# Kernel tuning notes

Measured on AMD Instinct MI355X. Metric: run time of the kernel, lower is better.

Reference implementation:

```python
import jax, jax.numpy as jnp
import numpy as np

B, N, T, S, H = 8, 10000, 2000, 12, 128
BIN_SIGMA = 0.1
GAUSS_NORM = 0.3989422804  # 1/sqrt(2*pi), as hard-coded in the source


def setup_inputs() -> dict:
    key = jax.random.key(0)
    ks = jax.random.split(key, 8)
    # (x, y, z): x,y in detector mm, z already expressed in waveform-tick units
    scale = jnp.array([400.0, 400.0, float(T - 1)], dtype=jnp.float32)
    diffused_electrons = jax.random.uniform(ks[0], (B, N, 3), dtype=jnp.float32) * scale
    mask = jax.random.uniform(ks[1], (B, N), dtype=jnp.float32)  # per-electron weights
    W1 = jax.random.normal(ks[2], (3, H), dtype=jnp.float32) * (1.0 / np.sqrt(3.0))
    b1 = jnp.zeros((H,), dtype=jnp.float32)
    W2 = jax.random.normal(ks[3], (H, H), dtype=jnp.float32) * (1.0 / np.sqrt(H))
    b2 = jnp.zeros((H,), dtype=jnp.float32)
    W3 = jax.random.normal(ks[4], (H, S), dtype=jnp.float32) * (1.0 / np.sqrt(H))
    b3 = jnp.zeros((S,), dtype=jnp.float32)
    return {"diffused_electrons": diffused_electrons, "mask": mask,
            "W1": W1, "b1": b1, "W2": W2, "b2": b2, "W3": W3, "b3": b3}


def _mlp(x, W1, b1, W2, b2, W3, b3):
    h = jax.nn.relu(x @ W1 + b1)
    h = jaxax = jax.nn.relu(h @ W2 + b2)
    return h @ W3 + b3


def reference(diffused_electrons, mask, W1, b1, W2, b2, W3, b3):
    # sensor_simulator: per-electron sensor response [B, N, S]
    h = jax.nn.relu(diffused_electrons @ W1 + b1)
    h = jax.nn.relu(h @ W2 + b2)
    response = h @ W3 + b3  # [B, N, S]

    z = diffused_electrons[:, :, 2]  # [B, N]
    ticks = jnp.arange(T, dtype=diffused_electrons.dtype)  # linspace(0, T-1, T)
    # Gaussian soft-binning kernel, [B, N, T] (the large HBM intermediate)
    d = ticks[None, None, :] - z[:, :, None]
    exp_values = jnp.exp(-(d * d) / (2.0 * BIN_SIGMA))
    exp_values = exp_values * (mask * (GAUSS_NORM / np.sqrt(BIN_SIGMA)))[:, :, None]
    # transpose().matmul(sensor_response) then transpose -> [B, S, T]
    waveforms = jnp.einsum('bnt,bns->bst', exp_values, response)
    return waveforms
```

## Files before the change

kernel.cpp:

```cpp
#include <hip/hip_runtime.h>
#include <hip/hip_fp16.h>

#define BB 8
#define NN 10000
#define TT 2000
#define SS 12
#define HH 128
#define TOTAL_E (BB * NN)
#define COEF 1.2615662610100802f

#define CAP 32
#define REC_W 8

#define TB 20
#define NB 26

#define WS_CURSOR 0
#define WS_REC    65536

typedef _Float16 half8 __attribute__((ext_vector_type(8)));
typedef float f32x4 __attribute__((ext_vector_type(4)));

__device__ __forceinline__ int swz(int row, int chunk) {
    return row * 128 + ((chunk ^ (row & 7)) * 8);
}

__global__ __launch_bounds__(256) void mlp_kernel(
    const float* __restrict__ de,
    const float* __restrict__ mask,
    const float* __restrict__ W1, const float* __restrict__ b1,
    const float* __restrict__ W2, const float* __restrict__ b2,
    const float* __restrict__ W3, const float* __restrict__ b3,
    unsigned int* __restrict__ cursor,
    float* __restrict__ rec)
{
    __shared__ _Float16 sW2T[HH * 128];
    __shared__ _Float16 sh[64 * 128];

    const int tid = threadIdx.x;
    const int wave = tid >> 6;
    const int lane = tid & 63;
    const int q = lane >> 4;
    const int i = lane & 15;

    {
        const int n = tid >> 1;
        const int kh = (tid & 1) * 8;
        #pragma unroll
        for (int c8 = 0; c8 < 8; ++c8) {
            const int c = kh + c8;
            half8 v;
            #pragma unroll
            for (int j = 0; j < 8; ++j)
                v[j] = (_Float16)W2[(c * 8 + j) * HH + n];
            *(half8*)(sW2T + swz(n, c)) = v;
        }
    }

    half8 bW1[8];
    #pragma unroll
    for (int nt = 0; nt < 8; ++nt) {
        half8 f = {};
        if (q == 0) {
            const int n = nt * 16 + i;
            f[0] = (_Float16)W1[n];
            f[1] = (_Float16)W1[HH + n];
            f[2] = (_Float16)W1[2 * HH + n];
        }
        bW1[nt] = f;
    }
    half8 bW3[4];
    #pragma unroll
    for (int c = 0; c < 4; ++c) {
        half8 f = {};
        if (i < SS) {
            #pragma unroll
            for (int j = 0; j < 8; ++j)
                f[j] = (_Float16)W3[(c * 32 + q * 8 + j) * SS + i];
        }
        bW3[c] = f;
    }
    float b1v[8], b2v[8];
    #pragma unroll
    for (int nt = 0; nt < 8; ++nt) {
        b1v[nt] = b1[nt * 16 + i];
        b2v[nt] = b2[nt * 16 + i];
    }
    const float b3v = (i < SS) ? b3[i] : 0.f;

    __syncthreads();

    const int mrow = wave * 16;

    for (int base = blockIdx.x * 64; base < TOTAL_E; base += gridDim.x * 64) {
        const int m_glob = base + mrow + i;
        const int bi = m_glob / NN;
        const float x0 = de[m_glob * 3 + 0];
        const float x1 = de[m_glob * 3 + 1];
        const float x2 = de[m_glob * 3 + 2];
        const float coef = mask[m_glob] * COEF;

        half8 aX = {};
        if (q == 0) { aX[0] = (_Float16)x0; aX[1] = (_Float16)x1; aX[2] = (_Float16)x2; }

        #pragma unroll
        for (int nt = 0; nt < 8; ++nt) {
            f32x4 acc = {};
            acc = __builtin_amdgcn_mfma_f32_16x16x32_f16(aX, bW1[nt], acc, 0, 0, 0);
            #pragma unroll
            for (int r = 0; r < 4; ++r) {
                float v = acc[r] + b1v[nt];
                v = v > 0.f ? v : 0.f;
                const int row = mrow + q * 4 + r;
                const int col = nt * 16 + i;
                sh[swz(row, col >> 3) + (col & 7)] = (_Float16)v;
            }
        }
        __syncthreads();

        half8 aH[4];
        #pragma unroll
        for (int c = 0; c < 4; ++c)
            aH[c] = *(const half8*)(sh + swz(mrow + i, c * 4 + q));
        __syncthreads();

        f32x4 acc2[8];
        #pragma unroll
        for (int nt = 0; nt < 8; ++nt) acc2[nt] = (f32x4){};
        #pragma unroll
        for (int nt = 0; nt < 8; ++nt) {
            #pragma unroll
            for (int c = 0; c < 4; ++c) {
                half8 bf = *(const half8*)(sW2T + swz(nt * 16 + i, c * 4 + q));
                acc2[nt] = __builtin_amdgcn_mfma_f32_16x16x32_f16(aH[c], bf, acc2[nt], 0, 0, 0);
            }
        }
        #pragma unroll
        for (int nt = 0; nt < 8; ++nt) {
            #pragma unroll
            for (int r = 0; r < 4; ++r) {
                float v = acc2[nt][r] + b2v[nt];
                v = v > 0.f ? v : 0.f;
                const int row = mrow + q * 4 + r;
                const int col = nt * 16 + i;
                sh[swz(row, col >> 3) + (col & 7)] = (_Float16)v;
            }
        }
        __syncthreads();

        f32x4 acc3 = {};
        #pragma unroll
        for (int c = 0; c < 4; ++c) {
            half8 a2 = *(const half8*)(sh + swz(mrow + i, c * 4 + q));
            acc3 = __builtin_amdgcn_mfma_f32_16x16x32_f16(a2, bW3[c], acc3, 0, 0, 0);
        }

        unsigned int ridx = 0;
        if (lane < 16) {
            int bin = (int)x2;
            bin = bin < 0 ? 0 : (bin > TT - 1 ? TT - 1 : bin);
            unsigned int slot = atomicAdd(&cursor[bi * TT + bin], 1u);
            if (slot >= CAP) slot = CAP - 1;
            ridx = (unsigned int)(bi * TT + bin) * CAP + slot;
        }

        #pragma unroll
        for (int r = 0; r < 4; ++r) {
            const int e = q * 4 + r;
            const unsigned int rx = __shfl(ridx, e);
            const float zr = __shfl(x2, e);
            const float cr = __shfl(coef, e);
            float val = acc3[r] + b3v;
            float val_hi = __shfl(val, lane + 1);
            float dv = 0.f;
            int f = -1;
            if (i < 12 && !(i & 1)) {
                __half2 h2;
                h2.x = __float2half(val);
                h2.y = __float2half(val_hi);
                dv = *(float*)&h2;
                f = 2 + (i >> 1);
            } else if (i == 12) { dv = zr; f = 0; }
            else if (i == 13)   { dv = cr; f = 1; }
            if (f >= 0)
                rec[(size_t)rx * REC_W + f] = dv;
        }
        __syncthreads();
    }
}

__global__ __launch_bounds__(256) void gather_kernel(
    const unsigned int* __restrict__ cursor,
    const float* __restrict__ rec,
    float* __restrict__ out)
{
    __shared__ float sz[NB * CAP];
    __shared__ float sc[NB * CAP];
    __shared__ unsigned int srsp[NB * CAP * 6];
    __shared__ unsigned int lcnt[NB];

    const int b = blockIdx.x / (TT / TB);
    const int t0 = (blockIdx.x % (TT / TB)) * TB;
    const int tid = threadIdx.x;
    const int wv = tid >> 6;
    const int ln = tid & 63;

    for (int bb = wv; bb < NB; bb += 4) {
        const int g = t0 - 3 + bb;
        unsigned int c = 0;
        if (g >= 0 && g < TT) {
            c = cursor[b * TT + g];
            if (c > CAP) c = CAP;
        }
        if (ln == 0) lcnt[bb] = c;
        const float* src = rec + (size_t)(b * TT + g) * CAP * REC_W;
        for (unsigned int idx = ln; idx < c * 8u; idx += 64) {
            const unsigned int slot = idx >> 3;
            const unsigned int w = idx & 7;
            const float v = src[slot * REC_W + w];
            const int ls = bb * CAP + slot;
            if (w == 0)      sz[ls] = v;
            else if (w == 1) sc[ls] = v;
            else             srsp[ls * 6 + (w - 2)] = __float_as_uint(v);
        }
    }
    __syncthreads();

    const int t_l = tid / SS;
    const int s = tid - t_l * SS;
    if (t_l >= TB) return;
    const int t = t0 + t_l;
    const float tf = (float)t;
    float acc = 0.f;
    #pragma unroll
    for (int o = 0; o < 7; ++o) {
        const int bb = t_l + o;
        const unsigned int c = lcnt[bb];
        const int base = bb * CAP;
        for (unsigned int u = 0; u < c; ++u) {
            const int ls = base + u;
            const float z = sz[ls];
            const float cc = sc[ls];
            const float d = tf - z;
            const unsigned int rw = srsp[ls * 6 + (s >> 1)];
            const __half2 h2 = *(const __half2*)&rw;
            const float rv = (s & 1) ? __half2float(h2.y) : __half2float(h2.x);
            acc = fmaf(__expf(-5.0f * d * d) * cc, rv, acc);
        }
    }
    out[(b * SS + s) * TT + t] = acc;
}

extern "C" void kernel_launch(void* const* d_in, const int* in_sizes, int n_in,
                              void* d_out, int out_size, void* d_ws, size_t ws_size,
                              hipStream_t stream) {
    const float* de   = (const float*)d_in[0];
    const float* mask = (const float*)d_in[1];
    const float* W1   = (const float*)d_in[2];
    const float* b1   = (const float*)d_in[3];
    const float* W2   = (const float*)d_in[4];
    const float* b2   = (const float*)d_in[5];
    const float* W3   = (const float*)d_in[6];
    const float* b3   = (const float*)d_in[7];
    float* out = (float*)d_out;

    char* ws = (char*)d_ws;
    unsigned int* cursor = (unsigned int*)(ws + WS_CURSOR);
    float*        rec    = (float*)(ws + WS_REC);

    hipMemsetAsync(cursor, 0, BB * TT * sizeof(unsigned int), stream);

    mlp_kernel<<<625, 256, 0, stream>>>(de, mask, W1, b1, W2, b2, W3, b3,
                                        cursor, rec);
    gather_kernel<<<BB * (TT / TB), 256, 0, stream>>>(cursor, rec, out);
}
```

Baseline: 105.3 us.

## Replace block barriers with wave fences, fold bias into MFMA, pad gather LDS

Result: faster. 103.1 us (-2.2%).

```diff
diff --git a/kernel.cpp b/kernel.cpp
--- a/kernel.cpp
+++ b/kernel.cpp
@@ -14,6 +14,8 @@
 
 #define TB 20
 #define NB 26
+#define SZP 33
+#define SRP 198
 
 #define WS_CURSOR 0
 #define WS_REC    65536
@@ -21,8 +23,21 @@
 typedef _Float16 half8 __attribute__((ext_vector_type(8)));
 typedef float f32x4 __attribute__((ext_vector_type(4)));
 
+#define WAVE_LDS_FENCE() do { \
+    __asm__ volatile("" ::: "memory"); \
+    __builtin_amdgcn_wave_barrier(); \
+    __asm__ volatile("" ::: "memory"); \
+} while (0)
+
 __device__ __forceinline__ int swz(int row, int chunk) {
     return row * 128 + ((chunk ^ (row & 7)) * 8);
+}
+
+__device__ __forceinline__ unsigned int pack2(float a, float b) {
+    _Float16 ha = (_Float16)a, hb = (_Float16)b;
+    unsigned short ua = __builtin_bit_cast(unsigned short, ha);
+    unsigned short ub = __builtin_bit_cast(unsigned short, hb);
+    return (unsigned int)ua | ((unsigned int)ub << 16);
 }
 
 __global__ __launch_bounds__(256) void mlp_kernel(
@@ -66,6 +81,7 @@
             f[0] = (_Float16)W1[n];
             f[1] = (_Float16)W1[HH + n];
             f[2] = (_Float16)W1[2 * HH + n];
+            f[3] = (_Float16)b1[n];
         }
         bW1[nt] = f;
     }
@@ -80,17 +96,21 @@
         }
         bW3[c] = f;
     }
-    float b1v[8], b2v[8];
-    #pragma unroll
-    for (int nt = 0; nt < 8; ++nt) {
-        b1v[nt] = b1[nt * 16 + i];
-        b2v[nt] = b2[nt * 16 + i];
-    }
-    const float b3v = (i < SS) ? b3[i] : 0.f;
+    float b2f[8][4];
+    #pragma unroll
+    for (int nt = 0; nt < 8; ++nt)
+        #pragma unroll
+        for (int r = 0; r < 4; ++r)
+            b2f[nt][r] = b2[nt * 16 + q * 4 + r];
+    float b3f[4];
+    #pragma unroll
+    for (int r = 0; r < 4; ++r)
+        b3f[r] = (q < 3) ? b3[q * 4 + r] : 0.f;
 
     __syncthreads();
 
     const int mrow = wave * 16;
+    const int hrow = mrow + i;
 
     for (int base = blockIdx.x * 64; base < TOTAL_E; base += gridDim.x * 64) {
         const int m_glob = base + mrow + i;
@@ -101,58 +121,60 @@
         const float coef = mask[m_glob] * COEF;
 
         half8 aX = {};
-        if (q == 0) { aX[0] = (_Float16)x0; aX[1] = (_Float16)x1; aX[2] = (_Float16)x2; }
+        if (q == 0) {
+            aX[0] = (_Float16)x0; aX[1] = (_Float16)x1;
+            aX[2] = (_Float16)x2; aX[3] = (_Float16)1.f;
+        }
+
+        WAVE_LDS_FENCE();
 
         #pragma unroll
         for (int nt = 0; nt < 8; ++nt) {
-            f32x4 acc = {};
-            acc = __builtin_amdgcn_mfma_f32_16x16x32_f16(aX, bW1[nt], acc, 0, 0, 0);
+            f32x4 a = {};
+            a = __builtin_amdgcn_mfma_f32_16x16x32_f16(bW1[nt], aX, a, 0, 0, 0);
+            const unsigned int lo = pack2(fmaxf(a[0], 0.f), fmaxf(a[1], 0.f));
+            const unsigned int hi = pack2(fmaxf(a[2], 0.f), fmaxf(a[3], 0.f));
+            const int chunk = nt * 2 + (q >> 1);
+            uint2 u; u.x = lo; u.y = hi;
+            *(uint2*)(sh + hrow * 128 + ((chunk ^ (i & 7)) * 8) + (q & 1) * 4) = u;
+        }
+        WAVE_LDS_FENCE();
+
+        half8 aH[4];
+        #pragma unroll
+        for (int c = 0; c < 4; ++c)
+            aH[c] = *(const half8*)(sh + swz(hrow, c * 4 + q));
+
+        f32x4 acc2[8];
+        #pragma unroll
+        for (int nt = 0; nt < 8; ++nt) acc2[nt] = (f32x4){};
+        #pragma unroll
+        for (int c = 0; c < 4; ++c) {
             #pragma unroll
-            for (int r = 0; r < 4; ++r) {
-                float v = acc[r] + b1v[nt];
-                v = v > 0.f ? v : 0.f;
-                const int row = mrow + q * 4 + r;
-                const int col = nt * 16 + i;
-                sh[swz(row, col >> 3) + (col & 7)] = (_Float16)v;
+            for (int nt = 0; nt < 8; ++nt) {
+                const half8 bf = *(const half8*)(sW2T + swz(nt * 16 + i, c * 4 + q));
+                acc2[nt] = __builtin_amdgcn_mfma_f32_16x16x32_f16(bf, aH[c], acc2[nt], 0, 0, 0);
             }
         }
-        __syncthreads();
-
-        half8 aH[4];
-        #pragma unroll
-        for (int c = 0; c < 4; ++c)
-            aH[c] = *(const half8*)(sh + swz(mrow + i, c * 4 + q));
-        __syncthreads();
-
-        f32x4 acc2[8];
-        #pragma unroll
-        for (int nt = 0; nt < 8; ++nt) acc2[nt] = (f32x4){};
+        WAVE_LDS_FENCE();
+
         #pragma unroll
         for (int nt = 0; nt < 8; ++nt) {
-            #pragma unroll
-            for (int c = 0; c < 4; ++c) {
-                half8 bf = *(const half8*)(sW2T + swz(nt * 16 + i, c * 4 + q));
-                acc2[nt] = __builtin_amdgcn_mfma_f32_16x16x32_f16(aH[c], bf, acc2[nt], 0, 0, 0);
-            }
-        }
-        #pragma unroll
-        for (int nt = 0; nt < 8; ++nt) {
-            #pragma unroll
-            for (int r = 0; r < 4; ++r) {
-                float v = acc2[nt][r] + b2v[nt];
-                v = v > 0.f ? v : 0.f;
-                const int row = mrow + q * 4 + r;
-                const int col = nt * 16 + i;
-                sh[swz(row, col >> 3) + (col & 7)] = (_Float16)v;
-            }
-        }
-        __syncthreads();
+            const unsigned int lo = pack2(fmaxf(acc2[nt][0] + b2f[nt][0], 0.f),
+                                          fmaxf(acc2[nt][1] + b2f[nt][1], 0.f));
+            const unsigned int hi = pack2(fmaxf(acc2[nt][2] + b2f[nt][2], 0.f),
+                                          fmaxf(acc2[nt][3] + b2f[nt][3], 0.f));
+            const int chunk = nt * 2 + (q >> 1);
+            uint2 u; u.x = lo; u.y = hi;
+            *(uint2*)(sh + hrow * 128 + ((chunk ^ (i & 7)) * 8) + (q & 1) * 4) = u;
+        }
+        WAVE_LDS_FENCE();
 
         f32x4 acc3 = {};
         #pragma unroll
         for (int c = 0; c < 4; ++c) {
-            half8 a2 = *(const half8*)(sh + swz(mrow + i, c * 4 + q));
-            acc3 = __builtin_amdgcn_mfma_f32_16x16x32_f16(a2, bW3[c], acc3, 0, 0, 0);
+            const half8 a2 = *(const half8*)(sh + swz(hrow, c * 4 + q));
+            acc3 = __builtin_amdgcn_mfma_f32_16x16x32_f16(bW3[c], a2, acc3, 0, 0, 0);
         }
 
         unsigned int ridx = 0;
@@ -163,29 +185,18 @@
             if (slot >= CAP) slot = CAP - 1;
             ridx = (unsigned int)(bi * TT + bin) * CAP + slot;
         }
-
-        #pragma unroll
-        for (int r = 0; r < 4; ++r) {
-            const int e = q * 4 + r;
-            const unsigned int rx = __shfl(ridx, e);
-            const float zr = __shfl(x2, e);
-            const float cr = __shfl(coef, e);
-            float val = acc3[r] + b3v;
-            float val_hi = __shfl(val, lane + 1);
-            float dv = 0.f;
-            int f = -1;
-            if (i < 12 && !(i & 1)) {
-                __half2 h2;
-                h2.x = __float2half(val);
-                h2.y = __float2half(val_hi);
-                dv = *(float*)&h2;
-                f = 2 + (i >> 1);
-            } else if (i == 12) { dv = zr; f = 0; }
-            else if (i == 13)   { dv = cr; f = 1; }
-            if (f >= 0)
-                rec[(size_t)rx * REC_W + f] = dv;
-        }
-        __syncthreads();
+        const unsigned int rx = (unsigned int)__shfl((int)ridx, i);
+
+        float2 v;
+        int off;
+        if (q == 3) {
+            v.x = x2; v.y = coef; off = 0;
+        } else {
+            v.x = __uint_as_float(pack2(acc3[0] + b3f[0], acc3[1] + b3f[1]));
+            v.y = __uint_as_float(pack2(acc3[2] + b3f[2], acc3[3] + b3f[3]));
+            off = 2 + 2 * q;
+        }
+        *(float2*)(rec + (size_t)rx * REC_W + off) = v;
     }
 }
 
@@ -194,9 +205,9 @@
     const float* __restrict__ rec,
     float* __restrict__ out)
 {
-    __shared__ float sz[NB * CAP];
-    __shared__ float sc[NB * CAP];
-    __shared__ unsigned int srsp[NB * CAP * 6];
+    __shared__ float sz[NB * SZP];
+    __shared__ float sc[NB * SZP];
+    __shared__ unsigned int srsp[NB * SRP];
     __shared__ unsigned int lcnt[NB];
 
     const int b = blockIdx.x / (TT / TB);
@@ -218,10 +229,9 @@
             const unsigned int slot = idx >> 3;
             const unsigned int w = idx & 7;
             const float v = src[slot * REC_W + w];
-            const int ls = bb * CAP + slot;
-            if (w == 0)      sz[ls] = v;
-            else if (w == 1) sc[ls] = v;
-            else             srsp[ls * 6 + (w - 2)] = __float_as_uint(v);
+            if (w == 0)      sz[bb * SZP + slot] = v;
+            else if (w == 1) sc[bb * SZP + slot] = v;
+            else             srsp[bb * SRP + slot * 6u + (w - 2u)] = __float_as_uint(v);
         }
     }
     __syncthreads();
@@ -236,13 +246,13 @@
     for (int o = 0; o < 7; ++o) {
         const int bb = t_l + o;
         const unsigned int c = lcnt[bb];
-        const int base = bb * CAP;
+        const int zb = bb * SZP;
+        const int rb = bb * SRP;
         for (unsigned int u = 0; u < c; ++u) {
-            const int ls = base + u;
-            const float z = sz[ls];
-            const float cc = sc[ls];
+            const float z = sz[zb + u];
+            const float cc = sc[zb + u];
             const float d = tf - z;
-            const unsigned int rw = srsp[ls * 6 + (s >> 1)];
+            const unsigned int rw = srsp[rb + u * 6u + (unsigned)(s >> 1)];
             const __half2 h2 = *(const __half2*)&rw;
             const float rv = (s & 1) ? __half2float(h2.y) : __half2float(h2.x);
             acc = fmaf(__expf(-5.0f * d * d) * cc, rv, acc);
```
